# Performance work log

Hardware: AMD Instinct MI355X
Metric: run time of the kernel (lower is better)

The kernel has to match this reference:

```python
import jax, jax.numpy as jnp
import numpy as np

MARGIN = 1.0
ALFA = 0.1


def setup_inputs() -> dict:
    key = jax.random.key(0)
    k1, k2 = jax.random.split(key)
    N, D, T = 262144, 128, 262144
    embeddings = jax.random.normal(k1, (N, D), dtype=jnp.float32)
    triplets = jax.random.randint(k2, (T, 3), 0, N, dtype=jnp.int64)
    return {"embeddings": embeddings, "triplets": triplets}


def _corr_loss(embeddings):
    # torch_cov(rowvar=False): columns are variables -> D x D covariance
    N, D = embeddings.shape
    m = embeddings - jnp.mean(embeddings, axis=0, keepdims=True)  # [N, D]
    cov = jnp.einsum('ni,nj->ij', m, m) / (N - 1)                 # [D, D]
    V = jnp.diagonal(cov)                                          # variances
    corr2 = (cov / jnp.sqrt(V[:, None] * V[None, :])) ** 2
    # strict lower triangle, n*(n-1)/2 elements, then mean
    tril = jnp.tril(jnp.ones((D, D), dtype=corr2.dtype), k=-1)
    return jnp.sum(corr2 * tril) / (D * (D - 1) / 2)


def _triplet_loss(embeddings, triplets):
    pivot = embeddings[triplets[:, 0]]
    positives = embeddings[triplets[:, 1]]
    negatives = embeddings[triplets[:, 2]]
    ap = jnp.sum((pivot - positives) ** 2, axis=1)
    an = jnp.sum((pivot - negatives) ** 2, axis=1)
    return jnp.mean(jax.nn.relu(ap - an + MARGIN))


def reference(embeddings, triplets):
    corr_loss = _corr_loss(embeddings)
    triplet_loss = _triplet_loss(embeddings, triplets)
    return triplet_loss + ALFA * corr_loss
```

## Files before the change

kernel.cpp:

```cpp
#include <hip/hip_runtime.h>

#define D 128
#define MARGIN 1.0f
#define ALFA 0.1f
#define KC 64

#define WS_TSUM   0
#define WS_GRAM   256
#define WS_COLSUM (WS_GRAM + D * D)
#define WS_ZERO   (WS_COLSUM + D)
#define WS_PART   16896
#define PART_STRIDE (D * D + D)

typedef __attribute__((ext_vector_type(8)))  short bf16x8;
typedef __attribute__((ext_vector_type(16))) float f32x16;

__device__ __forceinline__ unsigned short f2bf(float f) {
    unsigned u = __float_as_uint(f);
    u += 0x7FFFu + ((u >> 16) & 1u);
    return (unsigned short)(u >> 16);
}

template<bool ATOMIC>
__global__ __launch_bounds__(512, 4) void gram_mfma(const float* __restrict__ emb,
                                                    int rowsPerBlock,
                                                    float* __restrict__ ws) {
    __shared__ __align__(16) char lds[2][128 * 128];
    __shared__ float csred[D];

    const int tid = threadIdx.x;
    const int l   = tid & 63;
    const int w   = tid >> 6;
    const int r0  = blockIdx.x * rowsPerBlock;

    const int rT = w & 3;
    const int c0 = (w >> 2) * 2;

    f32x16 acc0 = {};
    f32x16 acc1 = {};
    float cs[4] = {0.f, 0.f, 0.f, 0.f};
    const int d0 = (tid & 31) * 4;

    auto stage = [&](int cc, int b) {
#pragma unroll
        for (int j = 0; j < 2; ++j) {
            const int k = j * 32 + (tid >> 5) * 2;
            const float* base = emb + (size_t)(r0 + cc * KC + k) * D + d0;
            float4 a  = *(const float4*)base;
            float4 bv = *(const float4*)(base + D);
#pragma unroll
            for (int i = 0; i < 4; ++i) {
                float av = ((const float*)&a)[i];
                float bb = ((const float*)&bv)[i];
                cs[i] += av + bb;
                unsigned slotp = (unsigned)(k >> 3) ^ (unsigned)((tid & 31) & 7);
                unsigned off = (unsigned)(d0 + i) * 128u + slotp * 16u + (unsigned)((k & 7) << 1);
                *(unsigned*)(&lds[b][off]) = (unsigned)f2bf(av) | ((unsigned)f2bf(bb) << 16);
            }
        }
    };

    auto frag = [&](int t, int kb, int b) -> bf16x8 {
        const int d = t * 32 + (l & 31);
        const int k = kb + (l >> 5) * 8;
        unsigned slotp = (unsigned)(k >> 3) ^ ((unsigned)(d >> 2) & 7u);
        return *(const bf16x8*)(&lds[b][(unsigned)d * 128u + slotp * 16u]);
    };

    const int nChunks = rowsPerBlock / KC;
    stage(0, 0);
    for (int cc = 0; cc < nChunks; ++cc) {
        const int b = cc & 1;
        __syncthreads();
        if (cc + 1 < nChunks) stage(cc + 1, b ^ 1);
#pragma unroll
        for (int kb = 0; kb < KC; kb += 16) {
            bf16x8 fr = frag(rT,     kb, b);
            bf16x8 f0 = frag(c0,     kb, b);
            bf16x8 f1 = frag(c0 + 1, kb, b);
            acc0 = __builtin_amdgcn_mfma_f32_32x32x16_bf16(fr, f0, acc0, 0, 0, 0);
            acc1 = __builtin_amdgcn_mfma_f32_32x32x16_bf16(fr, f1, acc1, 0, 0, 0);
        }
    }
    __syncthreads();

    if (tid < D) csred[tid] = 0.f;
    __syncthreads();
#pragma unroll
    for (int i = 0; i < 4; ++i) atomicAdd(&csred[d0 + i], cs[i]);
    __syncthreads();

    float* gram   = ATOMIC ? ws + WS_GRAM
                           : ws + WS_PART + (size_t)blockIdx.x * PART_STRIDE;
    float* colsum = ATOMIC ? ws + WS_COLSUM : gram + D * D;

    if (tid < D) {
        if (ATOMIC) atomicAdd(&colsum[tid], csred[tid]);
        else        colsum[tid] = csred[tid];
    }

    const int row_hi = (l >> 5) * 4;
    const int col    = l & 31;
#pragma unroll
    for (int reg = 0; reg < 16; ++reg) {
        const int row32 = (reg & 3) + 8 * (reg >> 2) + row_hi;
        const int gr    = (rT * 32 + row32) * D;
        if (ATOMIC) {
            atomicAdd(&gram[gr + c0 * 32 + col],        acc0[reg]);
            atomicAdd(&gram[gr + (c0 + 1) * 32 + col],  acc1[reg]);
        } else {
            gram[gr + c0 * 32 + col]       = acc0[reg];
            gram[gr + (c0 + 1) * 32 + col] = acc1[reg];
        }
    }
}

__global__ __launch_bounds__(256) void reduce_partials(float* __restrict__ ws, int P, int slices) {
    const int nIdxBlocks = (PART_STRIDE + 255) / 256;
    const int idx   = (blockIdx.x % nIdxBlocks) * 256 + threadIdx.x;
    const int slice = blockIdx.x / nIdxBlocks;
    if (idx >= PART_STRIDE) return;
    const int per = P / slices;
    const float* part = ws + WS_PART;
    float s = 0.f;
    const int p0 = slice * per;
#pragma unroll 8
    for (int p = 0; p < per; ++p)
        s += part[(size_t)(p0 + p) * PART_STRIDE + idx];
    if (idx < D * D) atomicAdd(&ws[WS_GRAM + idx], s);
    else             atomicAdd(&ws[WS_COLSUM + (idx - D * D)], s);
}

__device__ __forceinline__ float d2diff(float4 p, float4 q, float4 r) {
    float ax = p.x - q.x, ay = p.y - q.y, az = p.z - q.z, aw = p.w - q.w;
    float bx = p.x - r.x, by = p.y - r.y, bz = p.z - r.z, bw = p.w - r.w;
    return (ax * ax + ay * ay + az * az + aw * aw)
         - (bx * bx + by * by + bz * bz + bw * bw);
}

__global__ __launch_bounds__(256, 8) void triplet_kernel(const float* __restrict__ emb,
                                                         const int* __restrict__ trip,
                                                         int T,
                                                         float* __restrict__ ws) {
    const int tid = threadIdx.x;
    const int li  = tid & 31;
    const int hw  = (blockIdx.x * blockDim.x + tid) >> 5;
    const int NH  = (gridDim.x * blockDim.x) >> 5;

    float wsum = 0.f;

    for (int t = hw; t < T; t += 2 * NH) {
        const int t2 = t + NH;
        const int i0 = trip[3 * t], i1 = trip[3 * t + 1], i2 = trip[3 * t + 2];
        float4 pv = ((const float4*)(emb + (size_t)i0 * D))[li];
        float4 qv = ((const float4*)(emb + (size_t)i1 * D))[li];
        float4 rv = ((const float4*)(emb + (size_t)i2 * D))[li];

        const bool has2 = (t2 < T);
        float4 pv2, qv2, rv2;
        if (has2) {
            const int j0 = trip[3 * t2], j1 = trip[3 * t2 + 1], j2 = trip[3 * t2 + 2];
            pv2 = ((const float4*)(emb + (size_t)j0 * D))[li];
            qv2 = ((const float4*)(emb + (size_t)j1 * D))[li];
            rv2 = ((const float4*)(emb + (size_t)j2 * D))[li];
        }

        float s = d2diff(pv, qv, rv);
#pragma unroll
        for (int off = 16; off; off >>= 1) s += __shfl_xor(s, off, 64);
        if (li == 0) wsum += fmaxf(s + MARGIN, 0.f);

        if (has2) {
            float s2 = d2diff(pv2, qv2, rv2);
#pragma unroll
            for (int off = 16; off; off >>= 1) s2 += __shfl_xor(s2, off, 64);
            if (li == 0) wsum += fmaxf(s2 + MARGIN, 0.f);
        }
    }

    __shared__ float red[8];
    if (li == 0) red[tid >> 5] = wsum;
    __syncthreads();
    if (tid == 0) {
        float b = 0.f;
#pragma unroll
        for (int i = 0; i < 8; ++i) b += red[i];
        atomicAdd(&ws[WS_TSUM], b);
    }
}

__global__ __launch_bounds__(256) void finalize_kernel(const float* __restrict__ ws,
                                                       float* __restrict__ out,
                                                       int N, int T) {
    const float* gram   = ws + WS_GRAM;
    const float* colsum = ws + WS_COLSUM;

    __shared__ float V[D];
    __shared__ float red[256];

    const int tid = threadIdx.x;
    const float invN   = 1.0f / (float)N;
    const float invNm1 = 1.0f / (float)(N - 1);

    if (tid < D) {
        float m = colsum[tid] * invN;
        V[tid] = (gram[tid * D + tid] - (float)N * m * m) * invNm1;
    }
    __syncthreads();

    float local = 0.f;
    for (int idx = tid; idx < D * D; idx += 256) {
        int i = idx >> 7, j = idx & 127;
        if (j < i) {
            float mi  = colsum[i] * invN;
            float mj  = colsum[j] * invN;
            float cov = (gram[idx] - (float)N * mi * mj) * invNm1;
            local += cov * cov / (V[i] * V[j]);
        }
    }
    red[tid] = local;
    __syncthreads();
    for (int s = 128; s > 0; s >>= 1) {
        if (tid < s) red[tid] += red[tid + s];
        __syncthreads();
    }
    if (tid == 0) {
        float corr_mean = red[0] / ((float)D * (float)(D - 1) * 0.5f);
        out[0] = ws[WS_TSUM] / (float)T + ALFA * corr_mean;
    }
}

extern "C" void kernel_launch(void* const* d_in, const int* in_sizes, int n_in,
                              void* d_out, int out_size, void* d_ws, size_t ws_size,
                              hipStream_t stream) {
    const float* emb  = (const float*)d_in[0];
    const int*   trip = (const int*)d_in[1];
    float*       out  = (float*)d_out;
    float*       ws   = (float*)d_ws;

    const int N = in_sizes[0] / D;
    const int T = in_sizes[1] / 3;

    hipMemsetAsync(d_ws, 0, WS_ZERO * sizeof(float), stream);

    const size_t need512 = ((size_t)WS_PART + (size_t)512 * PART_STRIDE) * sizeof(float);
    const size_t need256 = ((size_t)WS_PART + (size_t)256 * PART_STRIDE) * sizeof(float);

    if (ws_size >= need512) {
        gram_mfma<false><<<512, 512, 0, stream>>>(emb, N / 512, ws);
        reduce_partials<<<65 * 8, 256, 0, stream>>>(ws, 512, 8);
    } else if (ws_size >= need256) {
        gram_mfma<false><<<256, 512, 0, stream>>>(emb, N / 256, ws);
        reduce_partials<<<65 * 8, 256, 0, stream>>>(ws, 256, 8);
    } else {
        gram_mfma<true><<<256, 512, 0, stream>>>(emb, N / 256, ws);
    }

    triplet_kernel<<<2048, 256, 0, stream>>>(emb, trip, T, ws);
    finalize_kernel<<<1, 256, 0, stream>>>(ws, out, N, T);
}
```

Before: 291.7 us.

## Fuse gram MFMA and triplet gather into one heterogeneous-block kernel

Merges the Gram/colsum MFMA kernel and the triplet-loss gather kernel into a single launch. The first GB blocks do the Gram work and the remaining blocks do triplets, so the compute-bound MFMA phase and the memory-bound gather phase can run at the same time and one launch and its tail are removed. The triplet path now loads four triplets per half-warp iteration for more memory-level parallelism, and reduce_partials uses 16 slices. The risk is that triplet blocks inherit the 512-thread, LDS-heavy launch bounds of the Gram path, which could limit occupancy for the gather work.

After: 275.3 us. 5.6% less time.

```diff
diff --git a/kernel.cpp b/kernel.cpp
--- a/kernel.cpp
+++ b/kernel.cpp
@@ -4,6 +4,8 @@
 #define MARGIN 1.0f
 #define ALFA 0.1f
 #define KC 64
+#define GB 512
+#define TBLK 1024
 
 #define WS_TSUM   0
 #define WS_GRAM   256
@@ -21,96 +23,147 @@
     return (unsigned short)(u >> 16);
 }
 
+__device__ __forceinline__ float d2diff(float4 p, float4 q, float4 r) {
+    float ax = p.x - q.x, ay = p.y - q.y, az = p.z - q.z, aw = p.w - q.w;
+    float bx = p.x - r.x, by = p.y - r.y, bz = p.z - r.z, bw = p.w - r.w;
+    return (ax * ax + ay * ay + az * az + aw * aw)
+         - (bx * bx + by * by + bz * bz + bw * bw);
+}
+
 template<bool ATOMIC>
-__global__ __launch_bounds__(512, 4) void gram_mfma(const float* __restrict__ emb,
-                                                    int rowsPerBlock,
-                                                    float* __restrict__ ws) {
+__global__ __launch_bounds__(512, 4) void fused_kernel(const float* __restrict__ emb,
+                                                       const int* __restrict__ trip,
+                                                       int rowsPerBlock, int T,
+                                                       float* __restrict__ ws) {
     __shared__ __align__(16) char lds[2][128 * 128];
     __shared__ float csred[D];
 
     const int tid = threadIdx.x;
-    const int l   = tid & 63;
-    const int w   = tid >> 6;
-    const int r0  = blockIdx.x * rowsPerBlock;
-
-    const int rT = w & 3;
-    const int c0 = (w >> 2) * 2;
-
-    f32x16 acc0 = {};
-    f32x16 acc1 = {};
-    float cs[4] = {0.f, 0.f, 0.f, 0.f};
-    const int d0 = (tid & 31) * 4;
-
-    auto stage = [&](int cc, int b) {
-#pragma unroll
-        for (int j = 0; j < 2; ++j) {
-            const int k = j * 32 + (tid >> 5) * 2;
-            const float* base = emb + (size_t)(r0 + cc * KC + k) * D + d0;
-            float4 a  = *(const float4*)base;
-            float4 bv = *(const float4*)(base + D);
-#pragma unroll
-            for (int i = 0; i < 4; ++i) {
-                float av = ((const float*)&a)[i];
-                float bb = ((const float*)&bv)[i];
-                cs[i] += av + bb;
-                unsigned slotp = (unsigned)(k >> 3) ^ (unsigned)((tid & 31) & 7);
-                unsigned off = (unsigned)(d0 + i) * 128u + slotp * 16u + (unsigned)((k & 7) << 1);
-                *(unsigned*)(&lds[b][off]) = (unsigned)f2bf(av) | ((unsigned)f2bf(bb) << 16);
-            }
-        }
-    };
-
-    auto frag = [&](int t, int kb, int b) -> bf16x8 {
-        const int d = t * 32 + (l & 31);
-        const int k = kb + (l >> 5) * 8;
-        unsigned slotp = (unsigned)(k >> 3) ^ ((unsigned)(d >> 2) & 7u);
-        return *(const bf16x8*)(&lds[b][(unsigned)d * 128u + slotp * 16u]);
-    };
-
-    const int nChunks = rowsPerBlock / KC;
-    stage(0, 0);
-    for (int cc = 0; cc < nChunks; ++cc) {
-        const int b = cc & 1;
-        __syncthreads();
-        if (cc + 1 < nChunks) stage(cc + 1, b ^ 1);
-#pragma unroll
-        for (int kb = 0; kb < KC; kb += 16) {
-            bf16x8 fr = frag(rT,     kb, b);
-            bf16x8 f0 = frag(c0,     kb, b);
-            bf16x8 f1 = frag(c0 + 1, kb, b);
-            acc0 = __builtin_amdgcn_mfma_f32_32x32x16_bf16(fr, f0, acc0, 0, 0, 0);
-            acc1 = __builtin_amdgcn_mfma_f32_32x32x16_bf16(fr, f1, acc1, 0, 0, 0);
-        }
-    }
-    __syncthreads();
-
-    if (tid < D) csred[tid] = 0.f;
-    __syncthreads();
-#pragma unroll
-    for (int i = 0; i < 4; ++i) atomicAdd(&csred[d0 + i], cs[i]);
-    __syncthreads();
-
-    float* gram   = ATOMIC ? ws + WS_GRAM
-                           : ws + WS_PART + (size_t)blockIdx.x * PART_STRIDE;
-    float* colsum = ATOMIC ? ws + WS_COLSUM : gram + D * D;
-
-    if (tid < D) {
-        if (ATOMIC) atomicAdd(&colsum[tid], csred[tid]);
-        else        colsum[tid] = csred[tid];
-    }
-
-    const int row_hi = (l >> 5) * 4;
-    const int col    = l & 31;
-#pragma unroll
-    for (int reg = 0; reg < 16; ++reg) {
-        const int row32 = (reg & 3) + 8 * (reg >> 2) + row_hi;
-        const int gr    = (rT * 32 + row32) * D;
-        if (ATOMIC) {
-            atomicAdd(&gram[gr + c0 * 32 + col],        acc0[reg]);
-            atomicAdd(&gram[gr + (c0 + 1) * 32 + col],  acc1[reg]);
-        } else {
-            gram[gr + c0 * 32 + col]       = acc0[reg];
-            gram[gr + (c0 + 1) * 32 + col] = acc1[reg];
+
+    if (blockIdx.x < GB) {
+        const int l   = tid & 63;
+        const int w   = tid >> 6;
+        const int r0  = blockIdx.x * rowsPerBlock;
+
+        const int rT = w & 3;
+        const int c0 = (w >> 2) * 2;
+
+        f32x16 acc0 = {};
+        f32x16 acc1 = {};
+        float cs[4] = {0.f, 0.f, 0.f, 0.f};
+        const int d0 = (tid & 31) * 4;
+
+        auto stage = [&](int cc, int b) {
+#pragma unroll
+            for (int j = 0; j < 2; ++j) {
+                const int k = j * 32 + (tid >> 5) * 2;
+                const float* base = emb + (size_t)(r0 + cc * KC + k) * D + d0;
+                float4 a  = *(const float4*)base;
+                float4 bv = *(const float4*)(base + D);
+#pragma unroll
+                for (int i = 0; i < 4; ++i) {
+                    float av = ((const float*)&a)[i];
+                    float bb = ((const float*)&bv)[i];
+                    cs[i] += av + bb;
+                    unsigned slotp = (unsigned)(k >> 3) ^ (unsigned)((tid & 31) & 7);
+                    unsigned off = (unsigned)(d0 + i) * 128u + slotp * 16u + (unsigned)((k & 7) << 1);
+                    *(unsigned*)(&lds[b][off]) = (unsigned)f2bf(av) | ((unsigned)f2bf(bb) << 16);
+                }
+            }
+        };
+
+        auto frag = [&](int t, int kb, int b) -> bf16x8 {
+            const int d = t * 32 + (l & 31);
+            const int k = kb + (l >> 5) * 8;
+            unsigned slotp = (unsigned)(k >> 3) ^ ((unsigned)(d >> 2) & 7u);
+            return *(const bf16x8*)(&lds[b][(unsigned)d * 128u + slotp * 16u]);
+        };
+
+        const int nChunks = rowsPerBlock / KC;
+        stage(0, 0);
+        for (int cc = 0; cc < nChunks; ++cc) {
+            const int b = cc & 1;
+            __syncthreads();
+            if (cc + 1 < nChunks) stage(cc + 1, b ^ 1);
+#pragma unroll
+            for (int kb = 0; kb < KC; kb += 16) {
+                bf16x8 fr = frag(rT,     kb, b);
+                bf16x8 f0 = frag(c0,     kb, b);
+                bf16x8 f1 = frag(c0 + 1, kb, b);
+                acc0 = __builtin_amdgcn_mfma_f32_32x32x16_bf16(fr, f0, acc0, 0, 0, 0);
+                acc1 = __builtin_amdgcn_mfma_f32_32x32x16_bf16(fr, f1, acc1, 0, 0, 0);
+            }
+        }
+        __syncthreads();
+
+        if (tid < D) csred[tid] = 0.f;
+        __syncthreads();
+#pragma unroll
+        for (int i = 0; i < 4; ++i) atomicAdd(&csred[d0 + i], cs[i]);
+        __syncthreads();
+
+        float* gram   = ATOMIC ? ws + WS_GRAM
+                               : ws + WS_PART + (size_t)blockIdx.x * PART_STRIDE;
+        float* colsum = ATOMIC ? ws + WS_COLSUM : gram + D * D;
+
+        if (tid < D) {
+            if (ATOMIC) atomicAdd(&colsum[tid], csred[tid]);
+            else        colsum[tid] = csred[tid];
+        }
+
+        const int row_hi = (l >> 5) * 4;
+        const int col    = l & 31;
+#pragma unroll
+        for (int reg = 0; reg < 16; ++reg) {
+            const int row32 = (reg & 3) + 8 * (reg >> 2) + row_hi;
+            const int gr    = (rT * 32 + row32) * D;
+            if (ATOMIC) {
+                atomicAdd(&gram[gr + c0 * 32 + col],       acc0[reg]);
+                atomicAdd(&gram[gr + (c0 + 1) * 32 + col], acc1[reg]);
+            } else {
+                gram[gr + c0 * 32 + col]       = acc0[reg];
+                gram[gr + (c0 + 1) * 32 + col] = acc1[reg];
+            }
+        }
+    } else {
+        const int li  = tid & 31;
+        const int hwl = tid >> 5;
+        const int hw  = (blockIdx.x - GB) * 16 + hwl;
+        const int NH  = TBLK * 16;
+
+        float wsum = 0.f;
+
+        for (int t0 = hw; t0 < T; t0 += 4 * NH) {
+            float4 P[4], Q[4], R[4];
+#pragma unroll
+            for (int k = 0; k < 4; ++k) {
+                const int t = t0 + k * NH;
+                if (t < T) {
+                    const int i0 = trip[3 * t], i1 = trip[3 * t + 1], i2 = trip[3 * t + 2];
+                    P[k] = ((const float4*)(emb + (size_t)i0 * D))[li];
+                    Q[k] = ((const float4*)(emb + (size_t)i1 * D))[li];
+                    R[k] = ((const float4*)(emb + (size_t)i2 * D))[li];
+                }
+            }
+#pragma unroll
+            for (int k = 0; k < 4; ++k) {
+                const int t = t0 + k * NH;
+                if (t < T) {
+                    float s = d2diff(P[k], Q[k], R[k]);
+#pragma unroll
+                    for (int off = 16; off; off >>= 1) s += __shfl_xor(s, off, 64);
+                    if (li == 0) wsum += fmaxf(s + MARGIN, 0.f);
+                }
+            }
+        }
+
+        if (li == 0) csred[hwl] = wsum;
+        __syncthreads();
+        if (tid == 0) {
+            float b = 0.f;
+#pragma unroll
+            for (int i = 0; i < 16; ++i) b += csred[i];
+            atomicAdd(&ws[WS_TSUM], b);
         }
     }
 }
@@ -131,64 +184,6 @@
     else             atomicAdd(&ws[WS_COLSUM + (idx - D * D)], s);
 }
 
-__device__ __forceinline__ float d2diff(float4 p, float4 q, float4 r) {
-    float ax = p.x - q.x, ay = p.y - q.y, az = p.z - q.z, aw = p.w - q.w;
-    float bx = p.x - r.x, by = p.y - r.y, bz = p.z - r.z, bw = p.w - r.w;
-    return (ax * ax + ay * ay + az * az + aw * aw)
-         - (bx * bx + by * by + bz * bz + bw * bw);
-}
-
-__global__ __launch_bounds__(256, 8) void triplet_kernel(const float* __restrict__ emb,
-                                                         const int* __restrict__ trip,
-                                                         int T,
-                                                         float* __restrict__ ws) {
-    const int tid = threadIdx.x;
-    const int li  = tid & 31;
-    const int hw  = (blockIdx.x * blockDim.x + tid) >> 5;
-    const int NH  = (gridDim.x * blockDim.x) >> 5;
-
-    float wsum = 0.f;
-
-    for (int t = hw; t < T; t += 2 * NH) {
-        const int t2 = t + NH;
-        const int i0 = trip[3 * t], i1 = trip[3 * t + 1], i2 = trip[3 * t + 2];
-        float4 pv = ((const float4*)(emb + (size_t)i0 * D))[li];
-        float4 qv = ((const float4*)(emb + (size_t)i1 * D))[li];
-        float4 rv = ((const float4*)(emb + (size_t)i2 * D))[li];
-
-        const bool has2 = (t2 < T);
-        float4 pv2, qv2, rv2;
-        if (has2) {
-            const int j0 = trip[3 * t2], j1 = trip[3 * t2 + 1], j2 = trip[3 * t2 + 2];
-            pv2 = ((const float4*)(emb + (size_t)j0 * D))[li];
-            qv2 = ((const float4*)(emb + (size_t)j1 * D))[li];
-            rv2 = ((const float4*)(emb + (size_t)j2 * D))[li];
-        }
-
-        float s = d2diff(pv, qv, rv);
-#pragma unroll
-        for (int off = 16; off; off >>= 1) s += __shfl_xor(s, off, 64);
-        if (li == 0) wsum += fmaxf(s + MARGIN, 0.f);
-
-        if (has2) {
-            float s2 = d2diff(pv2, qv2, rv2);
-#pragma unroll
-            for (int off = 16; off; off >>= 1) s2 += __shfl_xor(s2, off, 64);
-            if (li == 0) wsum += fmaxf(s2 + MARGIN, 0.f);
-        }
-    }
-
-    __shared__ float red[8];
-    if (li == 0) red[tid >> 5] = wsum;
-    __syncthreads();
-    if (tid == 0) {
-        float b = 0.f;
-#pragma unroll
-        for (int i = 0; i < 8; ++i) b += red[i];
-        atomicAdd(&ws[WS_TSUM], b);
-    }
-}
-
 __global__ __launch_bounds__(256) void finalize_kernel(const float* __restrict__ ws,
                                                        float* __restrict__ out,
                                                        int N, int T) {
@@ -243,19 +238,14 @@
 
     hipMemsetAsync(d_ws, 0, WS_ZERO * sizeof(float), stream);
 
-    const size_t need512 = ((size_t)WS_PART + (size_t)512 * PART_STRIDE) * sizeof(float);
-    const size_t need256 = ((size_t)WS_PART + (size_t)256 * PART_STRIDE) * sizeof(float);
-
-    if (ws_size >= need512) {
-        gram_mfma<false><<<512, 512, 0, stream>>>(emb, N / 512, ws);
-        reduce_partials<<<65 * 8, 256, 0, stream>>>(ws, 512, 8);
-    } else if (ws_size >= need256) {
-        gram_mfma<false><<<256, 512, 0, stream>>>(emb, N / 256, ws);
-        reduce_partials<<<65 * 8, 256, 0, stream>>>(ws, 256, 8);
+    const size_t needP = ((size_t)WS_PART + (size_t)GB * PART_STRIDE) * sizeof(float);
+
+    if (ws_size >= needP) {
+        fused_kernel<false><<<GB + TBLK, 512, 0, stream>>>(emb, trip, N / GB, T, ws);
+        reduce_partials<<<65 * 16, 256, 0, stream>>>(ws, GB, 16);
     } else {
-        gram_mfma<true><<<256, 512, 0, stream>>>(emb, N / 256, ws);
-    }
-
-    triplet_kernel<<<2048, 256, 0, stream>>>(emb, trip, T, ws);
+        fused_kernel<true><<<GB + TBLK, 512, 0, stream>>>(emb, trip, N / GB, T, ws);
+    }
+
     finalize_kernel<<<1, 256, 0, stream>>>(ws, out, N, T);
 }
```
